# Optimization experiments

Hardware: AMD Instinct MI355X
Metric: run time of the kernel (lower is better)

The kernel has to match this reference:

```python
import jax, jax.numpy as jnp
import numpy as np

SIGMA = 25.0
B = 4096            # number of graphs
N = 1048576         # total nodes across batch
FEAT = 44           # node feature dim
TED = 84            # t_embed_dim = 128 - 44


def setup_inputs() -> dict:
    key = jax.random.key(0)
    ks = jax.random.split(key, 12)
    # ragged graph sizes via sorted random cut points -> ptr of length B+1
    cuts = jnp.sort(jax.random.randint(ks[0], (B - 1,), 0, N))
    ptr = jnp.concatenate([jnp.zeros((1,), jnp.int32), cuts.astype(jnp.int32), jnp.full((1,), N, jnp.int32)])
    node_attr = jax.random.normal(ks[1], (N, FEAT), dtype=jnp.float32)
    t = jax.random.uniform(ks[2], (B,), dtype=jnp.float32, minval=1e-3, maxval=1.0)
    # GaussianFourierProjection buffer (requires_grad=False in torch)
    W_f = jax.random.normal(ks[3], (TED // 2,), dtype=jnp.float32) * 30.0
    # embed Linear 84->84
    embed_w = jax.random.normal(ks[4], (TED, TED), dtype=jnp.float32) / np.sqrt(TED)
    embed_b = jax.random.normal(ks[5], (TED,), dtype=jnp.float32) * 0.01
    # Linear chain 128->64->32->4 (torch convention: W [out, in])
    w0 = jax.random.normal(ks[6], (64, 128), dtype=jnp.float32) / np.sqrt(128)
    b0 = jax.random.normal(ks[7], (64,), dtype=jnp.float32) * 0.01
    w1 = jax.random.normal(ks[8], (32, 64), dtype=jnp.float32) / np.sqrt(64)
    b1 = jax.random.normal(ks[9], (32,), dtype=jnp.float32) * 0.01
    w2 = jax.random.normal(ks[10], (4, 32), dtype=jnp.float32) / np.sqrt(32)
    b2 = jax.random.normal(ks[11], (4,), dtype=jnp.float32) * 0.01
    return {"node_attr": node_attr, "t": t, "ptr": ptr, "W_f": W_f,
            "embed_w": embed_w, "embed_b": embed_b,
            "w0": w0, "b0": b0, "w1": w1, "b1": b1, "w2": w2, "b2": b2}


def reference(node_attr, t, ptr, W_f, embed_w, embed_b, w0, b0, w1, b1, w2, b2):
    swish = lambda x: x * jax.nn.sigmoid(x)
    # GaussianFourierProjection: [B, TED]
    x_proj = t[:, None] * W_f[None, :] * (2.0 * np.pi)
    t_emb = jnp.concatenate([jnp.sin(x_proj), jnp.cos(x_proj)], axis=-1)
    embed = swish(t_emb @ embed_w.T + embed_b)                      # [B, TED]
    # ragged broadcast: graph id per node (replaces the torch per-graph tile loop)
    seg = jnp.searchsorted(ptr, jnp.arange(node_attr.shape[0], dtype=ptr.dtype), side='right') - 1
    h = jnp.concatenate([node_attr, embed[seg]], axis=-1)           # [N, 128]
    h = swish(h @ w0.T + b0)                                        # [N, 64]
    h = swish(h @ w1.T + b1)                                        # [N, 32]
    h = swish(h @ w2.T + b2)                                        # [N, 4]
    std = jnp.sqrt((SIGMA ** (2.0 * t) - 1.0) / (2.0 * np.log(SIGMA)))  # [B]
    return h / std[seg][:, None]
```

## Files before the change

### kernel.cpp

```cpp
#include <hip/hip_runtime.h>
#include <hip/hip_fp16.h>

typedef _Float16 f16x8 __attribute__((ext_vector_type(8)));
typedef __fp16   fp16x2 __attribute__((ext_vector_type(2)));
typedef float f32x4 __attribute__((ext_vector_type(4)));

#define FEAT 44
#define TED  84
#define MT   128
#define WN   32
#define NBLK 768
#define BUFB 6144

__global__ void prep_all(const float* __restrict__ t_arr, const float* __restrict__ W_f,
                         const float* __restrict__ embed_w, const float* __restrict__ embed_b,
                         const float* __restrict__ w0, const float* __restrict__ b0,
                         const float* __restrict__ w1, const float* __restrict__ w2,
                         const int* __restrict__ gptr, int* __restrict__ seg, int do_seg,
                         float* __restrict__ emb0, float* __restrict__ inv_std,
                         _Float16* __restrict__ w0h, _Float16* __restrict__ w1h,
                         _Float16* __restrict__ w2h, int B) {
    int g   = blockIdx.x;
    int tid = threadIdx.x;
    if (g == B) {
        for (int i = tid; i < 64 * 64; i += 128) {
            int o = i >> 6, k = i & 63;
            w0h[i] = (k < FEAT) ? (_Float16)w0[o * 128 + k] : (_Float16)0.f;
        }
        for (int i = tid; i < 32 * 64; i += 128) w1h[i] = (_Float16)w1[i];
        for (int i = tid; i < 16 * 32; i += 128) w2h[i] = (i < 4 * 32) ? (_Float16)w2[i] : (_Float16)0.f;
        return;
    }
    if (do_seg) {
        int a = gptr[g], b = gptr[g + 1];
        for (int i = a + tid; i < b; i += 128) seg[i] = g;
    }
    __shared__ float temb[TED];
    __shared__ float ses[TED];
    float tv = t_arr[g];
    if (tid < TED) {
        int j   = (tid < TED / 2) ? tid : tid - TED / 2;
        float x = tv * W_f[j] * 6.283185307179586f;
        temb[tid] = (tid < TED / 2) ? sinf(x) : cosf(x);
    }
    __syncthreads();
    if (tid < TED) {
        const float* wr = embed_w + tid * TED;
        float s = embed_b[tid];
        #pragma unroll 4
        for (int j = 0; j < TED; ++j) s = fmaf(temb[j], wr[j], s);
        ses[tid] = s / (1.0f + __expf(-s));
    }
    if (tid == TED) {
        const float c = 6.437751649736401f;
        inv_std[g] = rsqrtf(expm1f(c * tv) / c);
    }
    __syncthreads();
    if (tid < 64) {
        const float* wr = w0 + tid * 128 + FEAT;
        float s = b0[tid];
        #pragma unroll 4
        for (int j = 0; j < TED; ++j) s = fmaf(ses[j], wr[j], s);
        emb0[g * 64 + tid] = s;
    }
}

__device__ __forceinline__ float swishf(float x) {
    float e = __builtin_amdgcn_exp2f(x * -1.4426950408889634f);
    return x * __builtin_amdgcn_rcpf(1.0f + e);
}

__device__ __forceinline__ int ubound(const int* __restrict__ p, int n, int v) {
    int lo = 0, hi = n;
    while (lo < hi) { int m = (lo + hi) >> 1; if (p[m] <= v) lo = m + 1; else hi = m; }
    return lo - 1;
}

__device__ __forceinline__ void stage_attr(const float* __restrict__ node_attr, int row0,
                                           const char* lim, char* dst, int lane) {
    const char* g = (const char*)node_attr + (size_t)row0 * (FEAT * 4);
    #pragma unroll
    for (int k = 0; k < 6; ++k) {
        const char* s = g + k * 1024 + lane * 16;
        if (s > lim) s = lim;
        __builtin_amdgcn_global_load_lds(
            (const __attribute__((address_space(1))) unsigned int*)s,
            (__attribute__((address_space(3))) unsigned int*)(dst + k * 1024),
            16, 0, 0);
    }
}

template<bool USE_SEG>
__global__ __launch_bounds__(256)
void scorenet_main(const float* __restrict__ node_attr,
                   const int* __restrict__ gptr, int B,
                   const int* __restrict__ seg_arr,
                   const float* __restrict__ emb0,
                   const float* __restrict__ inv_std_g,
                   const _Float16* __restrict__ w0h,
                   const _Float16* __restrict__ w1h,
                   const _Float16* __restrict__ w2h,
                   const float* __restrict__ b1,
                   const float* __restrict__ b2,
                   float* __restrict__ out, int ntiles, int nbytes_attr) {
    __shared__ __align__(16) char lds[2 * BUFB * 4];

    const int t    = threadIdx.x;
    const int lane = t & 63;
    const int wid  = t >> 6;
    const int lr   = lane & 15;
    const int lk   = lane >> 4;
    const char* lim = (const char*)node_attr + nbytes_attr - 16;

    if (blockIdx.x >= ntiles) return;
    const int stride = gridDim.x;

    f16x8 aw0[2][4];
    #pragma unroll
    for (int kt = 0; kt < 2; ++kt)
        #pragma unroll
        for (int mt = 0; mt < 4; ++mt)
            aw0[kt][mt] = *(const f16x8*)(w0h + (mt * 16 + lr) * 64 + kt * 32 + lk * 8);
    f16x8 aw1[2][2];
    #pragma unroll
    for (int kt = 0; kt < 2; ++kt)
        #pragma unroll
        for (int mt = 0; mt < 2; ++mt)
            aw1[kt][mt] = *(const f16x8*)(w1h + (mt * 16 + lr) * 64 + kt * 32 + lk * 8);
    f16x8 aw2 = *(const f16x8*)(w2h + lr * 32 + lk * 8);
    f32x4 bias1f[2];
    #pragma unroll
    for (int mt = 0; mt < 2; ++mt) {
        float4 bv = *(const float4*)(b1 + mt * 16 + lk * 4);
        bias1f[mt] = f32x4{bv.x, bv.y, bv.z, bv.w};
    }
    float4 b2vv = *(const float4*)b2;
    const f32x4 c2init = (lk == 0) ? f32x4{b2vv.x, b2vv.y, b2vv.z, b2vv.w} : f32x4{0.f, 0.f, 0.f, 0.f};

    char* buf_cur = lds + wid * (2 * BUFB);
    char* buf_nxt = buf_cur + BUFB;

    int tile = blockIdx.x;

    stage_attr(node_attr, tile * MT + wid * WN, lim, buf_cur, lane);
    int s0, s1, n0, n1;
    {
        int wb = tile * MT + wid * WN;
        if (USE_SEG) { s0 = seg_arr[wb + lr]; s1 = seg_arr[wb + 16 + lr]; }
        else { s0 = ubound(gptr, B + 1, wb + lr); s1 = ubound(gptr, B + 1, wb + 16 + lr); }
        int t1 = tile + stride; if (t1 >= ntiles) t1 = tile;
        int wb1 = t1 * MT + wid * WN;
        if (USE_SEG) { n0 = seg_arr[wb1 + lr]; n1 = seg_arr[wb1 + 16 + lr]; }
        else { n0 = ubound(gptr, B + 1, wb1 + lr); n1 = ubound(gptr, B + 1, wb1 + 16 + lr); }
    }

    while (tile < ntiles) {
        const int wb = tile * MT + wid * WN;
        int tp1 = tile + stride;     if (tp1 >= ntiles) tp1 = tile;
        int tp2 = tile + 2 * stride; if (tp2 >= ntiles) tp2 = tile;

        float is0 = inv_std_g[s0];
        float is1 = inv_std_g[s1];
        f32x4 acc0[4][2];
        #pragma unroll
        for (int mt = 0; mt < 4; ++mt) {
            acc0[mt][0] = *(const f32x4*)(emb0 + s0 * 64 + mt * 16 + lk * 4);
            acc0[mt][1] = *(const f32x4*)(emb0 + s1 * 64 + mt * 16 + lk * 4);
        }

        stage_attr(node_attr, tp1 * MT + wid * WN, lim, buf_nxt, lane);

        int m0, m1;
        {
            int wb2 = tp2 * MT + wid * WN;
            if (USE_SEG) { m0 = seg_arr[wb2 + lr]; m1 = seg_arr[wb2 + 16 + lr]; }
            else { m0 = ubound(gptr, B + 1, wb2 + lr); m1 = ubound(gptr, B + 1, wb2 + 16 + lr); }
        }

        asm volatile("s_waitcnt vmcnt(20)" ::: "memory");
        __builtin_amdgcn_sched_barrier(0);

        union u8 { fp16x2 h2[4]; f16x8 v; };
        f16x8 bf[2][2];
        #pragma unroll
        for (int nt = 0; nt < 2; ++nt) {
            const float4* rowp = (const float4*)(buf_cur + (nt * 16 + lr) * (FEAT * 4));
            float4 a = rowp[lk * 2];
            float4 b = rowp[lk * 2 + 1];
            float4 c = make_float4(0.f, 0.f, 0.f, 0.f);
            float4 d = make_float4(0.f, 0.f, 0.f, 0.f);
            if (lk == 0) { c = rowp[8]; d = rowp[9]; }
            else if (lk == 1) { c = rowp[10]; }
            u8 f0, f1;
            f0.h2[0] = __builtin_amdgcn_cvt_pkrtz(a.x, a.y);
            f0.h2[1] = __builtin_amdgcn_cvt_pkrtz(a.z, a.w);
            f0.h2[2] = __builtin_amdgcn_cvt_pkrtz(b.x, b.y);
            f0.h2[3] = __builtin_amdgcn_cvt_pkrtz(b.z, b.w);
            f1.h2[0] = __builtin_amdgcn_cvt_pkrtz(c.x, c.y);
            f1.h2[1] = __builtin_amdgcn_cvt_pkrtz(c.z, c.w);
            f1.h2[2] = __builtin_amdgcn_cvt_pkrtz(d.x, d.y);
            f1.h2[3] = __builtin_amdgcn_cvt_pkrtz(d.z, d.w);
            bf[nt][0] = f0.v;
            bf[nt][1] = f1.v;
        }

        #pragma unroll
        for (int kt = 0; kt < 2; ++kt)
            #pragma unroll
            for (int mt = 0; mt < 4; ++mt)
                #pragma unroll
                for (int nt = 0; nt < 2; ++nt)
                    acc0[mt][nt] = __builtin_amdgcn_mfma_f32_16x16x32_f16(aw0[kt][mt], bf[nt][kt], acc0[mt][nt], 0, 0, 0);

        #pragma unroll
        for (int mt = 0; mt < 4; ++mt)
            #pragma unroll
            for (int nt = 0; nt < 2; ++nt) {
                int j = nt * 16 + lr;
                union { fp16x2 h2[2]; uint2 u; } p;
                p.h2[0] = __builtin_amdgcn_cvt_pkrtz(swishf(acc0[mt][nt][0]), swishf(acc0[mt][nt][1]));
                p.h2[1] = __builtin_amdgcn_cvt_pkrtz(swishf(acc0[mt][nt][2]), swishf(acc0[mt][nt][3]));
                int addr = j * 128 + (mt * 16 + lk * 4) * 2;
                *(uint2*)(buf_cur + (addr ^ ((j & 7) << 4))) = p.u;
            }

        f32x4 acc1[2][2];
        #pragma unroll
        for (int mt = 0; mt < 2; ++mt) { acc1[mt][0] = bias1f[mt]; acc1[mt][1] = bias1f[mt]; }
        #pragma unroll
        for (int kt = 0; kt < 2; ++kt) {
            f16x8 bx[2];
            #pragma unroll
            for (int nt = 0; nt < 2; ++nt) {
                int j    = nt * 16 + lr;
                int addr = j * 128 + kt * 64 + lk * 16;
                bx[nt] = *(const f16x8*)(buf_cur + (addr ^ ((j & 7) << 4)));
            }
            #pragma unroll
            for (int mt = 0; mt < 2; ++mt)
                #pragma unroll
                for (int nt = 0; nt < 2; ++nt)
                    acc1[mt][nt] = __builtin_amdgcn_mfma_f32_16x16x32_f16(aw1[kt][mt], bx[nt], acc1[mt][nt], 0, 0, 0);
        }

        #pragma unroll
        for (int mt = 0; mt < 2; ++mt)
            #pragma unroll
            for (int nt = 0; nt < 2; ++nt) {
                int j = nt * 16 + lr;
                union { fp16x2 h2[2]; uint2 u; } p;
                p.h2[0] = __builtin_amdgcn_cvt_pkrtz(swishf(acc1[mt][nt][0]), swishf(acc1[mt][nt][1]));
                p.h2[1] = __builtin_amdgcn_cvt_pkrtz(swishf(acc1[mt][nt][2]), swishf(acc1[mt][nt][3]));
                int addr = 4096 + j * 64 + (mt * 16 + lk * 4) * 2;
                *(uint2*)(buf_cur + (addr ^ ((j & 3) << 4))) = p.u;
            }

        f32x4 acc2[2] = {c2init, c2init};
        #pragma unroll
        for (int nt = 0; nt < 2; ++nt) {
            int j    = nt * 16 + lr;
            int addr = 4096 + j * 64 + lk * 16;
            f16x8 bx = *(const f16x8*)(buf_cur + (addr ^ ((j & 3) << 4)));
            acc2[nt] = __builtin_amdgcn_mfma_f32_16x16x32_f16(aw2, bx, acc2[nt], 0, 0, 0);
        }
        if (lk == 0) {
            #pragma unroll
            for (int nt = 0; nt < 2; ++nt) {
                int j = nt * 16 + lr;
                float is = nt ? is1 : is0;
                float4 o;
                o.x = swishf(acc2[nt][0]) * is;
                o.y = swishf(acc2[nt][1]) * is;
                o.z = swishf(acc2[nt][2]) * is;
                o.w = swishf(acc2[nt][3]) * is;
                *(float4*)(out + (size_t)(wb + j) * 4) = o;
            }
        }

        { char* tmp = buf_cur; buf_cur = buf_nxt; buf_nxt = tmp; }
        s0 = n0; s1 = n1; n0 = m0; n1 = m1;
        tile += stride;
    }
}

extern "C" void kernel_launch(void* const* d_in, const int* in_sizes, int n_in,
                              void* d_out, int out_size, void* d_ws, size_t ws_size,
                              hipStream_t stream) {
    const float* node_attr = (const float*)d_in[0];
    const float* t_arr     = (const float*)d_in[1];
    const int*   gptr      = (const int*)d_in[2];
    const float* W_f       = (const float*)d_in[3];
    const float* embed_w   = (const float*)d_in[4];
    const float* embed_b   = (const float*)d_in[5];
    const float* w0        = (const float*)d_in[6];
    const float* b0        = (const float*)d_in[7];
    const float* w1        = (const float*)d_in[8];
    const float* b1        = (const float*)d_in[9];
    const float* w2        = (const float*)d_in[10];
    const float* b2        = (const float*)d_in[11];
    float* out = (float*)d_out;

    const int N = in_sizes[0] / FEAT;
    const int B = in_sizes[2] - 1;
    const int ntiles = N / MT;
    const int nbytes_attr = in_sizes[0] * 4;

    char* ws = (char*)d_ws;
    size_t off = 0;
    float*    emb0    = (float*)(ws + off); off += (size_t)B * 64 * sizeof(float);
    off = (off + 1023) & ~(size_t)1023;
    float*    inv_std = (float*)(ws + off); off += (size_t)B * sizeof(float);
    off = (off + 1023) & ~(size_t)1023;
    _Float16* w0h = (_Float16*)(ws + off);  off += 64 * 64 * sizeof(_Float16);
    _Float16* w1h = (_Float16*)(ws + off);  off += 32 * 64 * sizeof(_Float16);
    _Float16* w2h = (_Float16*)(ws + off);  off += 16 * 32 * sizeof(_Float16);
    off = (off + 1023) & ~(size_t)1023;
    int* seg = (int*)(ws + off);
    size_t need_with_seg = off + (size_t)N * sizeof(int);
    bool use_seg = (ws_size >= need_with_seg);

    const int grid = (ntiles < NBLK) ? ntiles : NBLK;

    prep_all<<<B + 1, 128, 0, stream>>>(t_arr, W_f, embed_w, embed_b, w0, b0, w1, w2,
                                        gptr, seg, use_seg ? 1 : 0,
                                        emb0, inv_std, w0h, w1h, w2h, B);
    if (use_seg) {
        scorenet_main<true><<<grid, 256, 0, stream>>>(node_attr, gptr, B, seg, emb0, inv_std,
                                                      w0h, w1h, w2h, b1, b2, out, ntiles, nbytes_attr);
    } else {
        scorenet_main<false><<<grid, 256, 0, stream>>>(node_attr, gptr, B, seg, emb0, inv_std,
                                                       w0h, w1h, w2h, b1, b2, out, ntiles, nbytes_attr);
    }
}
```

Measured before the change: 83.83 us.

## Prefetch per-graph embeddings, use packed fp16 swish, and retune the grid size

Replaces the fp32 swish on the first two layers with a packed half2 exp2/rcp variant that converts to fp16 before the activation. The per-graph emb0 rows and inv_std values are now loaded one tile ahead into registers, hiding their latency behind the current tile. The grid drops from 768 to 512 blocks with launch_bounds(256,2), and the address clamp is applied only to the last staged chunk. The fp16 activation loses precision, and the prefetched registers raise register pressure.

```diff
diff --git a/kernel.cpp b/kernel.cpp
--- a/kernel.cpp
+++ b/kernel.cpp
@@ -9,7 +9,7 @@
 #define TED  84
 #define MT   128
 #define WN   32
-#define NBLK 768
+#define NBLK 512
 #define BUFB 6144
 
 __global__ void prep_all(const float* __restrict__ t_arr, const float* __restrict__ W_f,
@@ -70,6 +70,14 @@
     return x * __builtin_amdgcn_rcpf(1.0f + e);
 }
 
+__device__ __forceinline__ unsigned swish2(float x0, float x1) {
+    fp16x2 xp = __builtin_amdgcn_cvt_pkrtz(x0, x1);
+    __half2 x = *reinterpret_cast<__half2*>(&xp);
+    __half2 e = h2exp2(__hmul2(x, __float2half2_rn(-1.4426950408889634f)));
+    __half2 r = __hmul2(x, h2rcp(__hadd2(__float2half2_rn(1.0f), e)));
+    return *reinterpret_cast<unsigned*>(&r);
+}
+
 __device__ __forceinline__ int ubound(const int* __restrict__ p, int n, int v) {
     int lo = 0, hi = n;
     while (lo < hi) { int m = (lo + hi) >> 1; if (p[m] <= v) lo = m + 1; else hi = m; }
@@ -82,7 +90,7 @@
     #pragma unroll
     for (int k = 0; k < 6; ++k) {
         const char* s = g + k * 1024 + lane * 16;
-        if (s > lim) s = lim;
+        if (k == 5 && s > lim) s = lim;
         __builtin_amdgcn_global_load_lds(
             (const __attribute__((address_space(1))) unsigned int*)s,
             (__attribute__((address_space(3))) unsigned int*)(dst + k * 1024),
@@ -91,7 +99,7 @@
 }
 
 template<bool USE_SEG>
-__global__ __launch_bounds__(256)
+__global__ __launch_bounds__(256, 2)
 void scorenet_main(const float* __restrict__ node_attr,
                    const int* __restrict__ gptr, int B,
                    const int* __restrict__ seg_arr,
@@ -143,15 +151,24 @@
     int tile = blockIdx.x;
 
     stage_attr(node_attr, tile * MT + wid * WN, lim, buf_cur, lane);
-    int s0, s1, n0, n1;
+    f32x4 pe0[4], pe1[4];
+    float pistd0, pistd1;
+    int n0, n1;
     {
         int wb = tile * MT + wid * WN;
-        if (USE_SEG) { s0 = seg_arr[wb + lr]; s1 = seg_arr[wb + 16 + lr]; }
-        else { s0 = ubound(gptr, B + 1, wb + lr); s1 = ubound(gptr, B + 1, wb + 16 + lr); }
+        int q0 = USE_SEG ? seg_arr[wb + lr]      : ubound(gptr, B + 1, wb + lr);
+        int q1 = USE_SEG ? seg_arr[wb + 16 + lr] : ubound(gptr, B + 1, wb + 16 + lr);
+        pistd0 = inv_std_g[q0];
+        pistd1 = inv_std_g[q1];
+        #pragma unroll
+        for (int mt = 0; mt < 4; ++mt) {
+            pe0[mt] = *(const f32x4*)(emb0 + q0 * 64 + mt * 16 + lk * 4);
+            pe1[mt] = *(const f32x4*)(emb0 + q1 * 64 + mt * 16 + lk * 4);
+        }
         int t1 = tile + stride; if (t1 >= ntiles) t1 = tile;
         int wb1 = t1 * MT + wid * WN;
-        if (USE_SEG) { n0 = seg_arr[wb1 + lr]; n1 = seg_arr[wb1 + 16 + lr]; }
-        else { n0 = ubound(gptr, B + 1, wb1 + lr); n1 = ubound(gptr, B + 1, wb1 + 16 + lr); }
+        n0 = USE_SEG ? seg_arr[wb1 + lr]      : ubound(gptr, B + 1, wb1 + lr);
+        n1 = USE_SEG ? seg_arr[wb1 + 16 + lr] : ubound(gptr, B + 1, wb1 + 16 + lr);
     }
 
     while (tile < ntiles) {
@@ -159,13 +176,18 @@
         int tp1 = tile + stride;     if (tp1 >= ntiles) tp1 = tile;
         int tp2 = tile + 2 * stride; if (tp2 >= ntiles) tp2 = tile;
 
-        float is0 = inv_std_g[s0];
-        float is1 = inv_std_g[s1];
+        float is0 = pistd0;
+        float is1 = pistd1;
         f32x4 acc0[4][2];
         #pragma unroll
+        for (int mt = 0; mt < 4; ++mt) { acc0[mt][0] = pe0[mt]; acc0[mt][1] = pe1[mt]; }
+
+        pistd0 = inv_std_g[n0];
+        pistd1 = inv_std_g[n1];
+        #pragma unroll
         for (int mt = 0; mt < 4; ++mt) {
-            acc0[mt][0] = *(const f32x4*)(emb0 + s0 * 64 + mt * 16 + lk * 4);
-            acc0[mt][1] = *(const f32x4*)(emb0 + s1 * 64 + mt * 16 + lk * 4);
+            pe0[mt] = *(const f32x4*)(emb0 + n0 * 64 + mt * 16 + lk * 4);
+            pe1[mt] = *(const f32x4*)(emb0 + n1 * 64 + mt * 16 + lk * 4);
         }
 
         stage_attr(node_attr, tp1 * MT + wid * WN, lim, buf_nxt, lane);
@@ -173,8 +195,8 @@
         int m0, m1;
         {
             int wb2 = tp2 * MT + wid * WN;
-            if (USE_SEG) { m0 = seg_arr[wb2 + lr]; m1 = seg_arr[wb2 + 16 + lr]; }
-            else { m0 = ubound(gptr, B + 1, wb2 + lr); m1 = ubound(gptr, B + 1, wb2 + 16 + lr); }
+            m0 = USE_SEG ? seg_arr[wb2 + lr]      : ubound(gptr, B + 1, wb2 + lr);
+            m1 = USE_SEG ? seg_arr[wb2 + 16 + lr] : ubound(gptr, B + 1, wb2 + 16 + lr);
         }
 
         asm volatile("s_waitcnt vmcnt(20)" ::: "memory");
@@ -217,11 +239,11 @@
             #pragma unroll
             for (int nt = 0; nt < 2; ++nt) {
                 int j = nt * 16 + lr;
-                union { fp16x2 h2[2]; uint2 u; } p;
-                p.h2[0] = __builtin_amdgcn_cvt_pkrtz(swishf(acc0[mt][nt][0]), swishf(acc0[mt][nt][1]));
-                p.h2[1] = __builtin_amdgcn_cvt_pkrtz(swishf(acc0[mt][nt][2]), swishf(acc0[mt][nt][3]));
+                uint2 u;
+                u.x = swish2(acc0[mt][nt][0], acc0[mt][nt][1]);
+                u.y = swish2(acc0[mt][nt][2], acc0[mt][nt][3]);
                 int addr = j * 128 + (mt * 16 + lk * 4) * 2;
-                *(uint2*)(buf_cur + (addr ^ ((j & 7) << 4))) = p.u;
+                *(uint2*)(buf_cur + (addr ^ ((j & 7) << 4))) = u;
             }
 
         f32x4 acc1[2][2];
@@ -248,11 +270,11 @@
             #pragma unroll
             for (int nt = 0; nt < 2; ++nt) {
                 int j = nt * 16 + lr;
-                union { fp16x2 h2[2]; uint2 u; } p;
-                p.h2[0] = __builtin_amdgcn_cvt_pkrtz(swishf(acc1[mt][nt][0]), swishf(acc1[mt][nt][1]));
-                p.h2[1] = __builtin_amdgcn_cvt_pkrtz(swishf(acc1[mt][nt][2]), swishf(acc1[mt][nt][3]));
+                uint2 u;
+                u.x = swish2(acc1[mt][nt][0], acc1[mt][nt][1]);
+                u.y = swish2(acc1[mt][nt][2], acc1[mt][nt][3]);
                 int addr = 4096 + j * 64 + (mt * 16 + lk * 4) * 2;
-                *(uint2*)(buf_cur + (addr ^ ((j & 3) << 4))) = p.u;
+                *(uint2*)(buf_cur + (addr ^ ((j & 3) << 4))) = u;
             }
 
         f32x4 acc2[2] = {c2init, c2init};
@@ -278,7 +300,7 @@
         }
 
         { char* tmp = buf_cur; buf_cur = buf_nxt; buf_nxt = tmp; }
-        s0 = n0; s1 = n1; n0 = m0; n1 = m1;
+        n0 = m0; n1 = m1;
         tile += stride;
     }
 }
```

Measured after the change: 86.49 us. 1.03x slower.
